# Kernel optimization log

Hardware: AMD Instinct MI355X
Metric: run time of the kernel (lower is better)

Reference implementation:

```python
import jax, jax.numpy as jnp
import numpy as np

N_NODES = 100000
N_EDGES = 640000
IN_CH = 128
HID = 128


def setup_inputs() -> dict:
    key = jax.random.key(0)
    k1, k2, k3, k4, k5 = jax.random.split(key, 5)
    z = jax.random.normal(k1, (N_NODES, IN_CH), dtype=jnp.float32)
    edge_index = jax.random.randint(k2, (2, N_EDGES), 0, N_NODES, dtype=jnp.int64)
    # Linear layers: stored as [in, out] for x @ W + b
    s1 = 1.0 / np.sqrt(2 * IN_CH)
    W1 = jax.random.uniform(k3, (2 * IN_CH, HID), minval=-s1, maxval=s1, dtype=jnp.float32)
    b1 = jnp.zeros((HID,), dtype=jnp.float32)
    s2 = 1.0 / np.sqrt(HID)
    W2 = jax.random.uniform(k4, (HID, 1), minval=-s2, maxval=s2, dtype=jnp.float32)
    b2 = jnp.zeros((1,), dtype=jnp.float32)
    return {"z": z, "edge_index": edge_index, "W1": W1, "b1": b1, "W2": W2, "b2": b2}


def reference(z, edge_index, W1, b1, W2, b2):
    # gather source/destination node embeddings and concat -> [E, 2*C]
    h = jnp.concatenate([z[edge_index[0]], z[edge_index[1]]], axis=-1)
    h = jax.nn.relu(h @ W1 + b1)  # [E, HID]; Dropout(0.2) is identity in eval
    out = h @ W2 + b2             # [E, 1]
    return out.squeeze(-1)        # [E]
```

## Files before the change

### kernel.cpp

```cpp
#include <hip/hip_runtime.h>
#include <hip/hip_bf16.h>

typedef short bf16x8 __attribute__((ext_vector_type(8)));
typedef float f32x4  __attribute__((ext_vector_type(4)));
typedef unsigned short u16;

static __device__ __forceinline__ u16 f2bf(float f) {
    unsigned u = __float_as_uint(f);
    u += 0x7FFFu + ((u >> 16) & 1u);
    return (u16)(u >> 16);
}
static __device__ __forceinline__ float bf2f(u16 b) {
    return __uint_as_float(((unsigned)b) << 16);
}
static __device__ __forceinline__ unsigned pack2(float lo, float hi) {
    return (unsigned)f2bf(lo) | ((unsigned)f2bf(hi) << 16);
}

__global__ void prep_w(const float* __restrict__ W1, u16* __restrict__ Wl) {
    int idx = blockIdx.x * 256 + threadIdx.x;
    if (idx >= 256 * 128) return;
    int r = idx >> 7;
    int q = idx & 127;
    int k = (r < 128) ? r : (r - 128);
    int c = (r < 128) ? q : (q + 128);
    Wl[c * 128 + k] = f2bf(W1[idx]);
}

#define BM 64
__global__ __launch_bounds__(256, 2) void node_gemm(
    const float* __restrict__ z,
    const u16*   __restrict__ Wl,
    const float* __restrict__ b1,
    u16*         __restrict__ PQ,
    int M, int ntiles)
{
    __shared__ char As[BM * 256];
    __shared__ char Cb[BM * 512];
    const int tid  = threadIdx.x;
    const int lane = tid & 63;
    const int wave = tid >> 6;
    const int g    = lane >> 4;
    const int ln   = lane & 15;
    const int c0   = wave * 64;

    int t = blockIdx.x;
    if (t >= ntiles) return;

    bf16x8 af[4][4];
    #pragma unroll
    for (int ks = 0; ks < 4; ++ks)
        #pragma unroll
        for (int ci = 0; ci < 4; ++ci)
            af[ks][ci] = *(const bf16x8*)(Wl + (c0 + ci * 16 + ln) * 128 + ks * 32 + g * 8);

    float4 bias[4];
    #pragma unroll
    for (int ci = 0; ci < 4; ++ci) {
        int col = c0 + ci * 16 + g * 4;
        bias[ci] = (col < 128) ? *(const float4*)(b1 + col)
                               : make_float4(0.f, 0.f, 0.f, 0.f);
    }

    float4 r[8];

    {
        int m0 = t * BM;
        #pragma unroll
        for (int i = 0; i < 8; ++i) {
            int ci = tid + i * 256, row = ci >> 5, c4 = ci & 31;
            r[i] = make_float4(0.f, 0.f, 0.f, 0.f);
            if (m0 + row < M)
                r[i] = *(const float4*)(z + (size_t)(m0 + row) * 128 + c4 * 4);
        }
        #pragma unroll
        for (int i = 0; i < 8; ++i) {
            int ci = tid + i * 256, row = ci >> 5, c4 = ci & 31;
            ushort4 b;
            b.x = f2bf(r[i].x); b.y = f2bf(r[i].y);
            b.z = f2bf(r[i].z); b.w = f2bf(r[i].w);
            *(ushort4*)(As + row * 256 + ((c4 * 8) ^ ((row & 7) << 4))) = b;
        }
    }
    __syncthreads();

    while (true) {
        int next = t + gridDim.x;
        bool have = (next < ntiles);

        if (have) {
            int m0 = next * BM;
            #pragma unroll
            for (int i = 0; i < 8; ++i) {
                int ci = tid + i * 256, row = ci >> 5, c4 = ci & 31;
                r[i] = make_float4(0.f, 0.f, 0.f, 0.f);
                if (m0 + row < M)
                    r[i] = *(const float4*)(z + (size_t)(m0 + row) * 128 + c4 * 4);
            }
        }

        f32x4 acc[4][4];
        #pragma unroll
        for (int mf = 0; mf < 4; ++mf)
            #pragma unroll
            for (int ci = 0; ci < 4; ++ci)
                acc[mf][ci] = (f32x4){0.f, 0.f, 0.f, 0.f};
        #pragma unroll
        for (int ks = 0; ks < 4; ++ks) {
            #pragma unroll
            for (int mf = 0; mf < 4; ++mf) {
                int row  = mf * 16 + ln;
                int byte = row * 256 + ((ks * 64 + g * 16) ^ ((row & 7) << 4));
                bf16x8 b = *(const bf16x8*)(As + byte);
                #pragma unroll
                for (int ci = 0; ci < 4; ++ci)
                    acc[mf][ci] = __builtin_amdgcn_mfma_f32_16x16x32_bf16(
                        af[ks][ci], b, acc[mf][ci], 0, 0, 0);
            }
        }

        #pragma unroll
        for (int mf = 0; mf < 4; ++mf) {
            int node = mf * 16 + ln;
            #pragma unroll
            for (int ci = 0; ci < 4; ++ci) {
                int col = c0 + ci * 16 + g * 4;
                uint2 w;
                w.x = pack2(acc[mf][ci][0] + bias[ci].x,
                            acc[mf][ci][1] + bias[ci].y);
                w.y = pack2(acc[mf][ci][2] + bias[ci].z,
                            acc[mf][ci][3] + bias[ci].w);
                *(uint2*)(Cb + node * 512 + ((col * 2) ^ ((node & 7) << 4))) = w;
            }
        }
        __syncthreads();

        {
            int m0 = t * BM;
            int chunk = tid & 31;
            int nb    = tid >> 5;
            #pragma unroll
            for (int it = 0; it < 8; ++it) {
                int node = it * 8 + nb;
                uint4 v = *(const uint4*)(Cb + node * 512 +
                                          ((chunk * 16) ^ ((node & 7) << 4)));
                if (m0 + node < M)
                    *(uint4*)(PQ + (size_t)(m0 + node) * 256 + chunk * 8) = v;
            }
        }

        if (have) {
            #pragma unroll
            for (int i = 0; i < 8; ++i) {
                int ci = tid + i * 256, row = ci >> 5, c4 = ci & 31;
                ushort4 b;
                b.x = f2bf(r[i].x); b.y = f2bf(r[i].y);
                b.z = f2bf(r[i].z); b.w = f2bf(r[i].w);
                *(ushort4*)(As + row * 256 + ((c4 * 8) ^ ((row & 7) << 4))) = b;
            }
        } else {
            break;
        }
        __syncthreads();
        t = next;
    }
}

__global__ __launch_bounds__(256) void edge_mlp(
    const int* __restrict__ ei,
    const u16* __restrict__ PQ,
    const float* __restrict__ W2,
    const float* __restrict__ b2,
    float* __restrict__ out,
    int E)
{
    int gid = blockIdx.x * 256 + threadIdx.x;
    int e0  = (gid >> 4) * 4;
    int sub = gid & 15;
    if (e0 >= E) return;

    float4 w2a = *(const float4*)(W2 + sub * 8);
    float4 w2b = *(const float4*)(W2 + sub * 8 + 4);
    float ww[8] = {w2a.x, w2a.y, w2a.z, w2a.w, w2b.x, w2b.y, w2b.z, w2b.w};
    float bias = b2[0];

    if (e0 + 3 < E) {
        int4 s = *(const int4*)(ei + e0);
        int4 d = *(const int4*)(ei + E + e0);
        uint4 p0 = *(const uint4*)(PQ + (size_t)s.x * 256 + sub * 8);
        uint4 p1 = *(const uint4*)(PQ + (size_t)s.y * 256 + sub * 8);
        uint4 p2 = *(const uint4*)(PQ + (size_t)s.z * 256 + sub * 8);
        uint4 p3 = *(const uint4*)(PQ + (size_t)s.w * 256 + sub * 8);
        uint4 q0 = *(const uint4*)(PQ + (size_t)d.x * 256 + 128 + sub * 8);
        uint4 q1 = *(const uint4*)(PQ + (size_t)d.y * 256 + 128 + sub * 8);
        uint4 q2 = *(const uint4*)(PQ + (size_t)d.z * 256 + 128 + sub * 8);
        uint4 q3 = *(const uint4*)(PQ + (size_t)d.w * 256 + 128 + sub * 8);

        float a0 = 0.f, a1 = 0.f, a2 = 0.f, a3 = 0.f;
        const u16* pu0 = (const u16*)&p0; const u16* qu0 = (const u16*)&q0;
        const u16* pu1 = (const u16*)&p1; const u16* qu1 = (const u16*)&q1;
        const u16* pu2 = (const u16*)&p2; const u16* qu2 = (const u16*)&q2;
        const u16* pu3 = (const u16*)&p3; const u16* qu3 = (const u16*)&q3;
        #pragma unroll
        for (int j = 0; j < 8; ++j) {
            a0 = fmaf(fmaxf(bf2f(pu0[j]) + bf2f(qu0[j]), 0.f), ww[j], a0);
            a1 = fmaf(fmaxf(bf2f(pu1[j]) + bf2f(qu1[j]), 0.f), ww[j], a1);
            a2 = fmaf(fmaxf(bf2f(pu2[j]) + bf2f(qu2[j]), 0.f), ww[j], a2);
            a3 = fmaf(fmaxf(bf2f(pu3[j]) + bf2f(qu3[j]), 0.f), ww[j], a3);
        }
        #pragma unroll
        for (int m = 1; m < 16; m <<= 1) {
            a0 += __shfl_xor(a0, m);
            a1 += __shfl_xor(a1, m);
            a2 += __shfl_xor(a2, m);
            a3 += __shfl_xor(a3, m);
        }
        if (sub == 0) {
            float4 o = make_float4(a0 + bias, a1 + bias, a2 + bias, a3 + bias);
            *(float4*)(out + e0) = o;
        }
    } else {
        for (int k = 0; k < 4; ++k) {
            int e = e0 + k;
            if (e >= E) break;
            int sn = ei[e], dn = ei[E + e];
            uint4 p = *(const uint4*)(PQ + (size_t)sn * 256 + sub * 8);
            uint4 q = *(const uint4*)(PQ + (size_t)dn * 256 + 128 + sub * 8);
            const u16* pu = (const u16*)&p; const u16* qu = (const u16*)&q;
            float a = 0.f;
            #pragma unroll
            for (int j = 0; j < 8; ++j)
                a = fmaf(fmaxf(bf2f(pu[j]) + bf2f(qu[j]), 0.f), ww[j], a);
            #pragma unroll
            for (int m = 1; m < 16; m <<= 1) a += __shfl_xor(a, m);
            if (sub == 0) out[e] = a + bias;
        }
    }
}

extern "C" void kernel_launch(void* const* d_in, const int* in_sizes, int n_in,
                              void* d_out, int out_size, void* d_ws, size_t ws_size,
                              hipStream_t stream) {
    const float* z  = (const float*)d_in[0];
    const int*   ei = (const int*)d_in[1];
    const float* W1 = (const float*)d_in[2];
    const float* b1 = (const float*)d_in[3];
    const float* W2 = (const float*)d_in[4];
    const float* b2 = (const float*)d_in[5];
    float* out = (float*)d_out;

    const int M = in_sizes[0] / 128;
    const int E = in_sizes[1] / 2;

    u16* Wl = (u16*)d_ws;
    u16* PQ = (u16*)((char*)d_ws + 65536);

    hipLaunchKernelGGL(prep_w, dim3(128), dim3(256), 0, stream, W1, Wl);

    int ntiles = (M + BM - 1) / BM;
    int gb = ntiles < 512 ? ntiles : 512;
    hipLaunchKernelGGL(node_gemm, dim3(gb), dim3(256), 0, stream,
                       z, Wl, b1, PQ, M, ntiles);

    int eb = ((E + 3) / 4 * 16 + 255) / 256;
    hipLaunchKernelGGL(edge_mlp, dim3(eb), dim3(256), 0, stream,
                       ei, PQ, W2, b2, out, E);
}
```

Baseline: 74.13 us.

## Bucket-sort edges by source node and split PQ into separate P/Q tables

Adds a per-call counting sort of edges by source-node bucket (histogram, scan, atomic scatter into packed 64-bit records), so the edge MLP gathers source rows with better cache locality. The edge kernel writes outputs through the stored edge index, and uses an XCD-style block swizzle. The node GEMM output is split into separate P and Q arrays, and its occupancy hint and grid cap are raised. The cost is four extra kernel launches, an extra pass over edge_index, a scattered 8-byte write per edge, and scattered output stores.

```diff
diff --git a/kernel.cpp b/kernel.cpp
--- a/kernel.cpp
+++ b/kernel.cpp
@@ -4,6 +4,7 @@
 typedef short bf16x8 __attribute__((ext_vector_type(8)));
 typedef float f32x4  __attribute__((ext_vector_type(4)));
 typedef unsigned short u16;
+typedef unsigned long long u64;
 
 static __device__ __forceinline__ u16 f2bf(float f) {
     unsigned u = __float_as_uint(f);
@@ -20,20 +21,65 @@
 __global__ void prep_w(const float* __restrict__ W1, u16* __restrict__ Wl) {
     int idx = blockIdx.x * 256 + threadIdx.x;
     if (idx >= 256 * 128) return;
-    int r = idx >> 7;
-    int q = idx & 127;
+    int r = idx >> 7, q = idx & 127;
     int k = (r < 128) ? r : (r - 128);
     int c = (r < 128) ? q : (q + 128);
     Wl[c * 128 + k] = f2bf(W1[idx]);
 }
 
+__global__ void zero_hist(int* __restrict__ hist, int n) {
+    int i = blockIdx.x * 256 + threadIdx.x;
+    if (i < n) hist[i] = 0;
+}
+
+__global__ __launch_bounds__(256) void e_hist(
+    const int* __restrict__ ei, int* __restrict__ hist, int E, int NB)
+{
+    __shared__ int h[2048];
+    for (int i = threadIdx.x; i < NB; i += 256) h[i] = 0;
+    __syncthreads();
+    for (int e = blockIdx.x * 256 + threadIdx.x; e < E; e += gridDim.x * 256)
+        atomicAdd(&h[ei[e] >> 6], 1);
+    __syncthreads();
+    for (int i = threadIdx.x; i < NB; i += 256)
+        if (h[i]) atomicAdd(&hist[i], h[i]);
+}
+
+__global__ __launch_bounds__(1024) void e_scan(
+    const int* __restrict__ hist, int* __restrict__ cursor, int NB)
+{
+    __shared__ int s[2048];
+    int t = threadIdx.x;
+    s[t]        = (t < NB)        ? hist[t]        : 0;
+    s[t + 1024] = (t + 1024 < NB) ? hist[t + 1024] : 0;
+    __syncthreads();
+    for (int off = 1; off < 2048; off <<= 1) {
+        int a0 = s[t]        + ((t >= off)        ? s[t - off]        : 0);
+        int a1 = s[t + 1024] + ((t + 1024 >= off) ? s[t + 1024 - off] : 0);
+        __syncthreads();
+        s[t] = a0; s[t + 1024] = a1;
+        __syncthreads();
+    }
+    if (t < NB)        cursor[t]        = (t == 0) ? 0 : s[t - 1];
+    if (t + 1024 < NB) cursor[t + 1024] = s[t + 1023];
+}
+
+__global__ __launch_bounds__(256) void e_scatter(
+    const int* __restrict__ ei, int* __restrict__ cursor,
+    u64* __restrict__ se, int E)
+{
+    for (int e = blockIdx.x * 256 + threadIdx.x; e < E; e += gridDim.x * 256) {
+        int s = ei[e], d = ei[E + e];
+        int pos = atomicAdd(&cursor[s >> 6], 1);
+        se[pos] = (u64)s | ((u64)d << 17) | ((u64)e << 34);
+    }
+}
+
 #define BM 64
-__global__ __launch_bounds__(256, 2) void node_gemm(
-    const float* __restrict__ z,
-    const u16*   __restrict__ Wl,
+__global__ __launch_bounds__(256, 3) void node_gemm(
+    const float* __restrict__ z, const u16* __restrict__ Wl,
     const float* __restrict__ b1,
-    u16*         __restrict__ PQ,
-    int M, int ntiles)
+    u16* __restrict__ P, u16* __restrict__ Q, int M, int ntiles)
 {
     __shared__ char As[BM * 256];
     __shared__ char Cb[BM * 512];
@@ -63,7 +109,6 @@
     }
 
     float4 r[8];
-
     {
         int m0 = t * BM;
         #pragma unroll
@@ -144,8 +189,12 @@
                 int node = it * 8 + nb;
                 uint4 v = *(const uint4*)(Cb + node * 512 +
                                           ((chunk * 16) ^ ((node & 7) << 4)));
-                if (m0 + node < M)
-                    *(uint4*)(PQ + (size_t)(m0 + node) * 256 + chunk * 8) = v;
+                if (m0 + node < M) {
+                    u16* dst = (chunk < 16)
+                        ? (P + (size_t)(m0 + node) * 128 + chunk * 8)
+                        : (Q + (size_t)(m0 + node) * 128 + (chunk - 16) * 8);
+                    *(uint4*)dst = v;
+                }
             }
         }
 
@@ -166,75 +215,107 @@
     }
 }
 
-__global__ __launch_bounds__(256) void edge_mlp(
+__global__ __launch_bounds__(256) void edge_mlp_sorted(
+    const u64* __restrict__ se,
+    const u16* __restrict__ P, const u16* __restrict__ Q,
+    const float* __restrict__ W2, const float* __restrict__ b2,
+    float* __restrict__ out, int E)
+{
+    int cpx = gridDim.x >> 3;
+    int swz = (blockIdx.x & 7) * cpx + (blockIdx.x >> 3);
+    int pos0 = swz * 64 + (threadIdx.x >> 4) * 4;
+    int sub  = threadIdx.x & 15;
+    if (pos0 >= E) return;
+
+    float4 w2a = *(const float4*)(W2 + sub * 8);
+    float4 w2b = *(const float4*)(W2 + sub * 8 + 4);
+    float ww[8] = {w2a.x, w2a.y, w2a.z, w2a.w, w2b.x, w2b.y, w2b.z, w2b.w};
+    float bias = b2[0];
+
+    if (pos0 + 3 < E) {
+        ulonglong2 A = *(const ulonglong2*)(se + pos0);
+        ulonglong2 B = *(const ulonglong2*)(se + pos0 + 2);
+        u64 v[4] = {A.x, A.y, B.x, B.y};
+        float a[4];
+        uint4 pv[4], qv[4];
+        #pragma unroll
+        for (int k = 0; k < 4; ++k) {
+            unsigned s = (unsigned)(v[k] & 0x1FFFF);
+            unsigned d = (unsigned)((v[k] >> 17) & 0x1FFFF);
+            pv[k] = *(const uint4*)(P + (size_t)s * 128 + sub * 8);
+            qv[k] = *(const uint4*)(Q + (size_t)d * 128 + sub * 8);
+        }
+        #pragma unroll
+        for (int k = 0; k < 4; ++k) {
+            const u16* pu = (const u16*)&pv[k];
+            const u16* qu = (const u16*)&qv[k];
+            float acc = 0.f;
+            #pragma unroll
+            for (int j = 0; j < 8; ++j)
+                acc = fmaf(fmaxf(bf2f(pu[j]) + bf2f(qu[j]), 0.f), ww[j], acc);
+            a[k] = acc;
+        }
+        #pragma unroll
+        for (int m = 1; m < 16; m <<= 1) {
+            a[0] += __shfl_xor(a[0], m);
+            a[1] += __shfl_xor(a[1], m);
+            a[2] += __shfl_xor(a[2], m);
+            a[3] += __shfl_xor(a[3], m);
+        }
+        if (sub == 0) {
+            #pragma unroll
+            for (int k = 0; k < 4; ++k)
+                out[(unsigned)(v[k] >> 34)] = a[k] + bias;
+        }
+    } else {
+        for (int k = 0; k < 4; ++k) {
+            int pos = pos0 + k;
+            if (pos >= E) break;
+            u64 v = se[pos];
+            unsigned s = (unsigned)(v & 0x1FFFF);
+            unsigned d = (unsigned)((v >> 17) & 0x1FFFF);
+            uint4 p = *(const uint4*)(P + (size_t)s * 128 + sub * 8);
+            uint4 q = *(const uint4*)(Q + (size_t)d * 128 + sub * 8);
+            const u16* pu = (const u16*)&p; const u16* qu = (const u16*)&q;
+            float acc = 0.f;
+            #pragma unroll
+            for (int j = 0; j < 8; ++j)
+                acc = fmaf(fmaxf(bf2f(pu[j]) + bf2f(qu[j]), 0.f), ww[j], acc);
+            #pragma unroll
+            for (int m = 1; m < 16; m <<= 1) acc += __shfl_xor(acc, m);
+            if (sub == 0) out[(unsigned)(v >> 34)] = acc + bias;
+        }
+    }
+}
+
+__global__ __launch_bounds__(256) void edge_mlp_flat(
     const int* __restrict__ ei,
-    const u16* __restrict__ PQ,
-    const float* __restrict__ W2,
-    const float* __restrict__ b2,
-    float* __restrict__ out,
-    int E)
+    const u16* __restrict__ P, const u16* __restrict__ Q,
+    const float* __restrict__ W2, const float* __restrict__ b2,
+    float* __restrict__ out, int E)
 {
     int gid = blockIdx.x * 256 + threadIdx.x;
     int e0  = (gid >> 4) * 4;
     int sub = gid & 15;
     if (e0 >= E) return;
-
     float4 w2a = *(const float4*)(W2 + sub * 8);
     float4 w2b = *(const float4*)(W2 + sub * 8 + 4);
     float ww[8] = {w2a.x, w2a.y, w2a.z, w2a.w, w2b.x, w2b.y, w2b.z, w2b.w};
     float bias = b2[0];
-
-    if (e0 + 3 < E) {
-        int4 s = *(const int4*)(ei + e0);
-        int4 d = *(const int4*)(ei + E + e0);
-        uint4 p0 = *(const uint4*)(PQ + (size_t)s.x * 256 + sub * 8);
-        uint4 p1 = *(const uint4*)(PQ + (size_t)s.y * 256 + sub * 8);
-        uint4 p2 = *(const uint4*)(PQ + (size_t)s.z * 256 + sub * 8);
-        uint4 p3 = *(const uint4*)(PQ + (size_t)s.w * 256 + sub * 8);
-        uint4 q0 = *(const uint4*)(PQ + (size_t)d.x * 256 + 128 + sub * 8);
-        uint4 q1 = *(const uint4*)(PQ + (size_t)d.y * 256 + 128 + sub * 8);
-        uint4 q2 = *(const uint4*)(PQ + (size_t)d.z * 256 + 128 + sub * 8);
-        uint4 q3 = *(const uint4*)(PQ + (size_t)d.w * 256 + 128 + sub * 8);
-
-        float a0 = 0.f, a1 = 0.f, a2 = 0.f, a3 = 0.f;
-        const u16* pu0 = (const u16*)&p0; const u16* qu0 = (const u16*)&q0;
-        const u16* pu1 = (const u16*)&p1; const u16* qu1 = (const u16*)&q1;
-        const u16* pu2 = (const u16*)&p2; const u16* qu2 = (const u16*)&q2;
-        const u16* pu3 = (const u16*)&p3; const u16* qu3 = (const u16*)&q3;
-        #pragma unroll
-        for (int j = 0; j < 8; ++j) {
-            a0 = fmaf(fmaxf(bf2f(pu0[j]) + bf2f(qu0[j]), 0.f), ww[j], a0);
-            a1 = fmaf(fmaxf(bf2f(pu1[j]) + bf2f(qu1[j]), 0.f), ww[j], a1);
-            a2 = fmaf(fmaxf(bf2f(pu2[j]) + bf2f(qu2[j]), 0.f), ww[j], a2);
-            a3 = fmaf(fmaxf(bf2f(pu3[j]) + bf2f(qu3[j]), 0.f), ww[j], a3);
-        }
-        #pragma unroll
-        for (int m = 1; m < 16; m <<= 1) {
-            a0 += __shfl_xor(a0, m);
-            a1 += __shfl_xor(a1, m);
-            a2 += __shfl_xor(a2, m);
-            a3 += __shfl_xor(a3, m);
-        }
-        if (sub == 0) {
-            float4 o = make_float4(a0 + bias, a1 + bias, a2 + bias, a3 + bias);
-            *(float4*)(out + e0) = o;
-        }
-    } else {
-        for (int k = 0; k < 4; ++k) {
-            int e = e0 + k;
-            if (e >= E) break;
-            int sn = ei[e], dn = ei[E + e];
-            uint4 p = *(const uint4*)(PQ + (size_t)sn * 256 + sub * 8);
-            uint4 q = *(const uint4*)(PQ + (size_t)dn * 256 + 128 + sub * 8);
-            const u16* pu = (const u16*)&p; const u16* qu = (const u16*)&q;
-            float a = 0.f;
-            #pragma unroll
-            for (int j = 0; j < 8; ++j)
-                a = fmaf(fmaxf(bf2f(pu[j]) + bf2f(qu[j]), 0.f), ww[j], a);
-            #pragma unroll
-            for (int m = 1; m < 16; m <<= 1) a += __shfl_xor(a, m);
-            if (sub == 0) out[e] = a + bias;
-        }
+    for (int k = 0; k < 4; ++k) {
+        int e = e0 + k;
+        if (e >= E) break;
+        int sn = ei[e], dn = ei[E + e];
+        uint4 p = *(const uint4*)(P + (size_t)sn * 128 + sub * 8);
+        uint4 q = *(const uint4*)(Q + (size_t)dn * 128 + sub * 8);
+        const u16* pu = (const u16*)&p; const u16* qu = (const u16*)&q;
+        float acc = 0.f;
+        #pragma unroll
+        for (int j = 0; j < 8; ++j)
+            acc = fmaf(fmaxf(bf2f(pu[j]) + bf2f(qu[j]), 0.f), ww[j], acc);
+        #pragma unroll
+        for (int m = 1; m < 16; m <<= 1) acc += __shfl_xor(acc, m);
+        if (sub == 0) out[e] = acc + bias;
     }
 }
 
@@ -251,18 +332,47 @@
 
     const int M = in_sizes[0] / 128;
     const int E = in_sizes[1] / 2;
-
-    u16* Wl = (u16*)d_ws;
-    u16* PQ = (u16*)((char*)d_ws + 65536);
+    const int NB = (M + 63) >> 6;
+
+    char* ws = (char*)d_ws;
+    u16* Wl     = (u16*)ws;
+    int* hist   = (int*)(ws + 65536);
+    int* cursor = (int*)(ws + 73728);
+    size_t pOff = 81920;
+    size_t pqBytes = (size_t)M * 128 * 2;
+    u16* P = (u16*)(ws + pOff);
+    u16* Q = (u16*)(ws + pOff + pqBytes);
+    u64* se = (u64*)(ws + pOff + 2 * pqBytes);
+    size_t need = pOff + 2 * pqBytes + (size_t)E * 8;
+    bool do_sort = (ws_size >= need) && (NB <= 2048) && (M < (1 << 17)) &&
+                   (E < (1 << 20));
 
     hipLaunchKernelGGL(prep_w, dim3(128), dim3(256), 0, stream, W1, Wl);
 
+    if (do_sort) {
+        hipLaunchKernelGGL(zero_hist, dim3((NB + 255) / 256), dim3(256), 0,
+                           stream, hist, NB);
+        hipLaunchKernelGGL(e_hist, dim3(256), dim3(256), 0, stream,
+                           ei, hist, E, NB);
+        hipLaunchKernelGGL(e_scan, dim3(1), dim3(1024), 0, stream,
+                           hist, cursor, NB);
+        hipLaunchKernelGGL(e_scatter, dim3(256), dim3(256), 0, stream,
+                           ei, cursor, se, E);
+    }
+
     int ntiles = (M + BM - 1) / BM;
-    int gb = ntiles < 512 ? ntiles : 512;
+    int gb = ntiles < 768 ? ntiles : 768;
     hipLaunchKernelGGL(node_gemm, dim3(gb), dim3(256), 0, stream,
-                       z, Wl, b1, PQ, M, ntiles);
-
-    int eb = ((E + 3) / 4 * 16 + 255) / 256;
-    hipLaunchKernelGGL(edge_mlp, dim3(eb), dim3(256), 0, stream,
-                       ei, PQ, W2, b2, out, E);
-}
+                       z, Wl, b1, P, Q, M, ntiles);
+
+    if (do_sort) {
+        int nwg = (E + 63) / 64;
+        nwg = (nwg + 7) & ~7;
+        hipLaunchKernelGGL(edge_mlp_sorted, dim3(nwg), dim3(256), 0, stream,
+                           se, P, Q, W2, b2, out, E);
+    } else {
+        int eb = ((E + 3) / 4 * 16 + 255) / 256;
+        hipLaunchKernelGGL(edge_mlp_flat, dim3(eb), dim3(256), 0, stream,
+                           ei, P, Q, W2, b2, out, E);
+    }
+}
```

Result: slower. 234.0 us (+215.7%).
